# Kernel tuning notes

Measured on AMD Instinct MI355X. Metric: run time of the kernel, lower is better.

The kernel has to match this reference:

```python
import jax, jax.numpy as jnp
import numpy as np

B, A, C = 8, 150000, 10
ALPHA, GAMMA = 0.25, 2.0
STD = jnp.array([[0.1, 0.1, 0.2, 0.2]], dtype=jnp.float32)


def setup_inputs() -> dict:
    key = jax.random.key(0)
    ks = jax.random.split(key, 9)
    # ground-truth boxes (one per image), centered around (400,400)
    cx = jax.random.uniform(ks[0], (B,), minval=350., maxval=450.)
    cy = jax.random.uniform(ks[1], (B,), minval=350., maxval=450.)
    w = jax.random.uniform(ks[2], (B,), minval=80., maxval=180.)
    h = jax.random.uniform(ks[3], (B,), minval=80., maxval=180.)
    boxes = jnp.stack([cx - 0.5 * w, cy - 0.5 * h, cx + 0.5 * w, cy + 0.5 * h], axis=1)
    labels = (jax.random.uniform(ks[4], (B, C)) < 0.3).astype(jnp.float32)
    annotations = jnp.concatenate([boxes, labels], axis=1)  # [B, 4+C]
    n_near = A // 20
    kc = jax.random.split(ks[5], 4)
    ncx = jax.random.uniform(kc[0], (n_near,), minval=350., maxval=450.)
    ncy = jax.random.uniform(kc[1], (n_near,), minval=350., maxval=450.)
    nw = jax.random.uniform(kc[2], (n_near,), minval=80., maxval=180.)
    nh = jax.random.uniform(kc[3], (n_near,), minval=80., maxval=180.)
    kr = jax.random.split(ks[6], 4)
    rcx = jax.random.uniform(kr[0], (A - n_near,), minval=0., maxval=800.)
    rcy = jax.random.uniform(kr[1], (A - n_near,), minval=0., maxval=800.)
    rw = jax.random.uniform(kr[2], (A - n_near,), minval=20., maxval=300.)
    rh = jax.random.uniform(kr[3], (A - n_near,), minval=20., maxval=300.)
    acx = jnp.concatenate([ncx, rcx]); acy = jnp.concatenate([ncy, rcy])
    aw = jnp.concatenate([nw, rw]); ah = jnp.concatenate([nh, rh])
    anchors = jnp.stack([acx - 0.5 * aw, acy - 0.5 * ah, acx + 0.5 * aw, acy + 0.5 * ah], axis=1)[None]  # [1,A,4]
    attributes = jax.random.uniform(ks[7], (B, A, C), dtype=jnp.float32)  # probs in (0,1)
    regressions = jax.random.normal(ks[8], (B, A, 4), dtype=jnp.float32)
    return {"attributes": attributes, "regressions": regressions,
            "anchors": anchors, "annotations": annotations}


def reference(attributes, regressions, anchors, annotations):
    anchor = anchors[0]  # [A,4]
    aw = anchor[:, 2] - anchor[:, 0]
    ah = anchor[:, 3] - anchor[:, 1]
    acx = anchor[:, 0] + 0.5 * aw
    acy = anchor[:, 1] + 0.5 * ah

    def per_image(attribute, regression, ann):  # [A,C], [A,4], [4+C]
        box, labels = ann[:4], ann[4:]
        attribute = jnp.clip(attribute, 1e-4, 1.0 - 1e-4)
        # IoU of every anchor with the single gt box -> [A]
        area = (box[2] - box[0]) * (box[3] - box[1])
        iw = jnp.clip(jnp.minimum(anchor[:, 2], box[2]) - jnp.maximum(anchor[:, 0], box[0]), 0.0)
        ih = jnp.clip(jnp.minimum(anchor[:, 3], box[3]) - jnp.maximum(anchor[:, 1], box[1]), 0.0)
        inter = iw * ih
        union = jnp.clip(aw * ah + area - inter, 1e-8)
        iou = inter / union
        neg = iou < 0.4
        pos = iou >= 0.5
        num_pos = pos.sum()
        # classification targets: -1 ignore, 0 background, gt labels for positives
        targets = jnp.full(attribute.shape, -1.0, attribute.dtype)
        targets = jnp.where(neg[:, None], 0.0, targets)
        targets = jnp.where(pos[:, None], labels[None, :], targets)
        alpha_factor = jnp.where(targets == 1.0, ALPHA, 1.0 - ALPHA)
        focal_w = jnp.where(targets == 1.0, 1.0 - attribute, attribute)
        focal_w = alpha_factor * focal_w ** GAMMA
        bce = -(targets * jnp.log(attribute) + (1.0 - targets) * jnp.log(1.0 - attribute))
        att_loss = jnp.where(targets != -1.0, focal_w * bce, 0.0)
        att_loss = att_loss.sum() / jnp.maximum(num_pos.astype(attribute.dtype), 1.0)
        gw_raw = box[2] - box[0]; gh_raw = box[3] - box[1]
        gcx = box[0] + 0.5 * gw_raw; gcy = box[1] + 0.5 * gh_raw
        gw = jnp.clip(gw_raw, 1.0); gh = jnp.clip(gh_raw, 1.0)
        t = jnp.stack([(gcx - acx) / aw, (gcy - acy) / ah,
                       jnp.log(gw / aw), jnp.log(gh / ah)], axis=1) / STD  # [A,4]
        diff = jnp.abs(t - regression)
        rl = jnp.where(diff <= 1.0 / 9.0, 0.5 * 9.0 * diff ** 2, diff - 0.5 / 9.0)
        rl_sum = jnp.where(pos[:, None], rl, 0.0).sum()
        denom = jnp.maximum(num_pos, 1).astype(attribute.dtype) * 4.0  # mean over [P,4]
        reg_loss = jnp.where(num_pos > 0, rl_sum / denom, 0.0)
        return att_loss, reg_loss

    att_losses, reg_losses = jax.vmap(per_image)(attributes, regressions, annotations)
    return (att_losses.mean(keepdims=True), reg_losses.mean(keepdims=True))
```

## Files before the change

kernel.cpp:

```cpp
#include <hip/hip_runtime.h>

constexpr int B_IMG = 8;
constexpr int A_ANCH = 150000;
constexpr int C_CLS = 10;
constexpr int TPB = 256;
constexpr int NBX = (A_ANCH + TPB * 2 - 1) / (TPB * 2);

__global__ __launch_bounds__(TPB, 4) void focal_main(
    const float* __restrict__ attr,
    const float* __restrict__ regr,
    const float* __restrict__ anch,
    const float* __restrict__ ann,
    float* __restrict__ att_part,
    float* __restrict__ rl_part,
    float* __restrict__ np_part)
{
    const int b = blockIdx.y;
    const int a0 = (blockIdx.x * TPB + threadIdx.x) * 2;
    const bool valid = (a0 < A_ANCH);

    float4 at4[5];
    float4 an4[2];
    if (valid) {
        const float4* ap = reinterpret_cast<const float4*>(attr + ((size_t)b * A_ANCH + a0) * C_CLS);
#pragma unroll
        for (int j = 0; j < 5; ++j) at4[j] = ap[j];
        const float4* anp = reinterpret_cast<const float4*>(anch) + a0;
        an4[0] = anp[0];
        an4[1] = anp[1];
    }
    __builtin_amdgcn_sched_barrier(0);

    const float* annb = ann + b * 14;
    const float bx0 = annb[0], by0 = annb[1], bx1 = annb[2], by1 = annb[3];
    float lab[C_CLS];
#pragma unroll
    for (int c = 0; c < C_CLS; ++c) lab[c] = annb[4 + c];

    const float gw_raw = bx1 - bx0;
    const float gh_raw = by1 - by0;
    const float area = gw_raw * gh_raw;
    const float gcx = bx0 + 0.5f * gw_raw;
    const float gcy = by0 + 0.5f * gh_raw;
    const float gw = fmaxf(gw_raw, 1.0f);
    const float gh = fmaxf(gh_raw, 1.0f);

    const float TH  = (float)(1.0 / 9.0);
    const float SUB = (float)(0.5 / 9.0);
    const float PHI = (float)(1.0 - 0.0001);

    float att_sum = 0.0f;
    float rl_sum = 0.0f;
    float npf = 0.0f;

    if (valid) {
#pragma unroll
        for (int k = 0; k < 2; ++k) {
            const float ax0 = an4[k].x, ay0 = an4[k].y, ax1 = an4[k].z, ay1 = an4[k].w;
            const float aw = ax1 - ax0;
            const float ah = ay1 - ay0;
            float iw = fminf(ax1, bx1) - fmaxf(ax0, bx0);
            float ih = fminf(ay1, by1) - fmaxf(ay0, by0);
            iw = fmaxf(iw, 0.0f);
            ih = fmaxf(ih, 0.0f);
            const float inter = iw * ih;
            const float uni = fmaxf(aw * ah + area - inter, 1e-8f);
            const float iou = inter / uni;
            const bool pos = (iou >= 0.5f);
            const bool neg = (iou < 0.4f);

            if (pos || neg) {
#pragma unroll
                for (int c = 0; c < C_CLS; ++c) {
                    const int e = k * C_CLS + c;
                    const float4& v = at4[e >> 2];
                    const float pe = (e & 3) == 0 ? v.x : (e & 3) == 1 ? v.y : (e & 3) == 2 ? v.z : v.w;
                    const float p = fminf(fmaxf(pe, 1e-4f), PHI);
                    const float tgt = pos ? lab[c] : 0.0f;
                    float loss;
                    if (tgt == 1.0f) {
                        const float q = 1.0f - p;
                        loss = 0.25f * (q * q) * (-__logf(p));
                    } else {
                        loss = 0.75f * (p * p) * (-__logf(1.0f - p));
                    }
                    att_sum += loss;
                }
            }
            if (pos) {
                npf += 1.0f;
                const float acx = ax0 + 0.5f * aw;
                const float acy = ay0 + 0.5f * ah;
                const float t0 = ((gcx - acx) / aw) / 0.1f;
                const float t1 = ((gcy - acy) / ah) / 0.1f;
                const float t2 = __logf(gw / aw) / 0.2f;
                const float t3 = __logf(gh / ah) / 0.2f;
                const float4 r = *reinterpret_cast<const float4*>(regr + ((size_t)b * A_ANCH + a0 + k) * 4);
                float d;
                d = fabsf(t0 - r.x); rl_sum += (d <= TH) ? 4.5f * d * d : d - SUB;
                d = fabsf(t1 - r.y); rl_sum += (d <= TH) ? 4.5f * d * d : d - SUB;
                d = fabsf(t2 - r.z); rl_sum += (d <= TH) ? 4.5f * d * d : d - SUB;
                d = fabsf(t3 - r.w); rl_sum += (d <= TH) ? 4.5f * d * d : d - SUB;
            }
        }
    }

#pragma unroll
    for (int off = 32; off > 0; off >>= 1) {
        att_sum += __shfl_down(att_sum, off);
        rl_sum  += __shfl_down(rl_sum, off);
        npf     += __shfl_down(npf, off);
    }

    __shared__ float s_att[TPB / 64];
    __shared__ float s_rl[TPB / 64];
    __shared__ float s_np[TPB / 64];
    const int wave = threadIdx.x >> 6;
    const int lane = threadIdx.x & 63;
    if (lane == 0) { s_att[wave] = att_sum; s_rl[wave] = rl_sum; s_np[wave] = npf; }
    __syncthreads();
    if (threadIdx.x == 0) {
        float a0s = 0.0f, r0 = 0.0f, n0 = 0.0f;
#pragma unroll
        for (int w = 0; w < TPB / 64; ++w) { a0s += s_att[w]; r0 += s_rl[w]; n0 += s_np[w]; }
        const int idx = b * NBX + blockIdx.x;
        att_part[idx] = a0s;
        rl_part[idx]  = r0;
        np_part[idx]  = n0;
    }
}

__global__ __launch_bounds__(512) void focal_finalize(
    const float* __restrict__ att_part,
    const float* __restrict__ rl_part,
    const float* __restrict__ np_part,
    float* __restrict__ out)
{
    const int wave = threadIdx.x >> 6;
    const int lane = threadIdx.x & 63;
    float as = 0.0f, rs = 0.0f, ns = 0.0f;
    if (wave < B_IMG) {
        for (int i = lane; i < NBX; i += 64) {
            as += att_part[wave * NBX + i];
            rs += rl_part[wave * NBX + i];
            ns += np_part[wave * NBX + i];
        }
    }
#pragma unroll
    for (int off = 32; off > 0; off >>= 1) {
        as += __shfl_down(as, off);
        rs += __shfl_down(rs, off);
        ns += __shfl_down(ns, off);
    }
    __shared__ float sa[B_IMG], sr[B_IMG], sn[B_IMG];
    if (lane == 0 && wave < B_IMG) { sa[wave] = as; sr[wave] = rs; sn[wave] = ns; }
    __syncthreads();
    if (threadIdx.x == 0) {
        double am = 0.0, rm = 0.0;
        for (int b = 0; b < B_IMG; ++b) {
            const double npd = (double)sn[b];
            const double npf = npd > 0.0 ? npd : 1.0;
            am += (double)sa[b] / npf;
            if (npd > 0.0) rm += (double)sr[b] / (npf * 4.0);
        }
        out[0] = (float)(am / (double)B_IMG);
        out[1] = (float)(rm / (double)B_IMG);
    }
}

extern "C" void kernel_launch(void* const* d_in, const int* in_sizes, int n_in,
                              void* d_out, int out_size, void* d_ws, size_t ws_size,
                              hipStream_t stream) {
    const float* attr = (const float*)d_in[0];
    const float* regr = (const float*)d_in[1];
    const float* anch = (const float*)d_in[2];
    const float* ann  = (const float*)d_in[3];
    float* out = (float*)d_out;

    float* att_part = (float*)d_ws;
    float* rl_part  = att_part + B_IMG * NBX;
    float* np_part  = rl_part + B_IMG * NBX;

    dim3 grid(NBX, B_IMG);
    focal_main<<<grid, TPB, 0, stream>>>(attr, regr, anch, ann, att_part, rl_part, np_part);
    focal_finalize<<<1, 512, 0, stream>>>(att_part, rl_part, np_part, out);
}
```

Before: 23.52 us.

## Process four images per block with software-prefetched attribute loads

Each thread now handles the same two anchors across four images, loading the anchor boxes once and reusing their derived geometry. Attribute loads for the next image are double-buffered so they are in flight while the current image is computed. The block-level shared-memory reduction is dropped in favour of per-wave partial sums, and the finalize kernel reads the larger partial buffer. This cuts the grid to a quarter of its former size and raises register pressure, which may lower occupancy.

```diff
diff --git a/kernel.cpp b/kernel.cpp
--- a/kernel.cpp
+++ b/kernel.cpp
@@ -4,9 +4,14 @@
 constexpr int A_ANCH = 150000;
 constexpr int C_CLS = 10;
 constexpr int TPB = 256;
-constexpr int NBX = (A_ANCH + TPB * 2 - 1) / (TPB * 2);
-
-__global__ __launch_bounds__(TPB, 4) void focal_main(
+constexpr int BA = TPB * 2;
+constexpr int NBX = (A_ANCH + BA - 1) / BA;
+constexpr int IPG = 4;
+constexpr int NGRP = B_IMG / IPG;
+constexpr int WPB = TPB / 64;
+constexpr int SEG = NBX * WPB;
+
+__global__ __launch_bounds__(TPB) void focal_main(
     const float* __restrict__ attr,
     const float* __restrict__ regr,
     const float* __restrict__ anch,
@@ -15,118 +20,143 @@
     float* __restrict__ rl_part,
     float* __restrict__ np_part)
 {
-    const int b = blockIdx.y;
-    const int a0 = (blockIdx.x * TPB + threadIdx.x) * 2;
+    const int g   = blockIdx.y;
+    const int b0  = g * IPG;
+    const int tid = threadIdx.x;
+    const int a0  = (blockIdx.x * TPB + tid) * 2;
     const bool valid = (a0 < A_ANCH);
-
-    float4 at4[5];
-    float4 an4[2];
-    if (valid) {
-        const float4* ap = reinterpret_cast<const float4*>(attr + ((size_t)b * A_ANCH + a0) * C_CLS);
-#pragma unroll
-        for (int j = 0; j < 5; ++j) at4[j] = ap[j];
-        const float4* anp = reinterpret_cast<const float4*>(anch) + a0;
-        an4[0] = anp[0];
-        an4[1] = anp[1];
-    }
-    __builtin_amdgcn_sched_barrier(0);
-
-    const float* annb = ann + b * 14;
-    const float bx0 = annb[0], by0 = annb[1], bx1 = annb[2], by1 = annb[3];
-    float lab[C_CLS];
-#pragma unroll
-    for (int c = 0; c < C_CLS; ++c) lab[c] = annb[4 + c];
-
-    const float gw_raw = bx1 - bx0;
-    const float gh_raw = by1 - by0;
-    const float area = gw_raw * gh_raw;
-    const float gcx = bx0 + 0.5f * gw_raw;
-    const float gcy = by0 + 0.5f * gh_raw;
-    const float gw = fmaxf(gw_raw, 1.0f);
-    const float gh = fmaxf(gh_raw, 1.0f);
 
     const float TH  = (float)(1.0 / 9.0);
     const float SUB = (float)(0.5 / 9.0);
     const float PHI = (float)(1.0 - 0.0001);
 
-    float att_sum = 0.0f;
-    float rl_sum = 0.0f;
-    float npf = 0.0f;
+    float att[IPG], rl[IPG], npf[IPG];
+#pragma unroll
+    for (int i = 0; i < IPG; ++i) { att[i] = 0.0f; rl[i] = 0.0f; npf[i] = 0.0f; }
 
     if (valid) {
-#pragma unroll
-        for (int k = 0; k < 2; ++k) {
-            const float ax0 = an4[k].x, ay0 = an4[k].y, ax1 = an4[k].z, ay1 = an4[k].w;
-            const float aw = ax1 - ax0;
-            const float ah = ay1 - ay0;
-            float iw = fminf(ax1, bx1) - fmaxf(ax0, bx0);
-            float ih = fminf(ay1, by1) - fmaxf(ay0, by0);
-            iw = fmaxf(iw, 0.0f);
-            ih = fmaxf(ih, 0.0f);
-            const float inter = iw * ih;
-            const float uni = fmaxf(aw * ah + area - inter, 1e-8f);
-            const float iou = inter / uni;
-            const bool pos = (iou >= 0.5f);
-            const bool neg = (iou < 0.4f);
-
-            if (pos || neg) {
-#pragma unroll
-                for (int c = 0; c < C_CLS; ++c) {
-                    const int e = k * C_CLS + c;
-                    const float4& v = at4[e >> 2];
-                    const float pe = (e & 3) == 0 ? v.x : (e & 3) == 1 ? v.y : (e & 3) == 2 ? v.z : v.w;
-                    const float p = fminf(fmaxf(pe, 1e-4f), PHI);
-                    const float tgt = pos ? lab[c] : 0.0f;
-                    float loss;
-                    if (tgt == 1.0f) {
-                        const float q = 1.0f - p;
-                        loss = 0.25f * (q * q) * (-__logf(p));
-                    } else {
-                        loss = 0.75f * (p * p) * (-__logf(1.0f - p));
+        const float4* anp = reinterpret_cast<const float4*>(anch) + a0;
+        const float4 anA = anp[0];
+        const float4 anB = anp[1];
+        float ax1[2], ay1[2], aw[2], ah[2], acx[2], acy[2], aarea[2];
+        {
+            const float4 an[2] = {anA, anB};
+#pragma unroll
+            for (int k = 0; k < 2; ++k) {
+                ax1[k] = an[k].z; ay1[k] = an[k].w;
+                aw[k] = an[k].z - an[k].x;
+                ah[k] = an[k].w - an[k].y;
+                acx[k] = an[k].x + 0.5f * aw[k];
+                acy[k] = an[k].y + 0.5f * ah[k];
+                aarea[k] = aw[k] * ah[k];
+            }
+        }
+        const float ax0v[2] = {anA.x, anB.x};
+        const float ay0v[2] = {anA.y, anB.y};
+
+        const size_t f4row0 = (((size_t)b0 * A_ANCH + a0) * C_CLS) >> 2;
+        const size_t f4stride = ((size_t)A_ANCH * C_CLS) >> 2;
+        const float4* atp = reinterpret_cast<const float4*>(attr);
+
+        float4 bufA[5], bufB[5];
+#pragma unroll
+        for (int j = 0; j < 5; ++j) bufA[j] = atp[f4row0 + j];
+
+        auto body = [&](const int i, float4 (&cur)[5], float4 (&nxt)[5],
+                        const bool prefetch, float& att_i, float& rl_i, float& np_i) {
+            const int b = b0 + i;
+            if (prefetch) {
+#pragma unroll
+                for (int j = 0; j < 5; ++j) nxt[j] = atp[f4row0 + (size_t)(i + 1) * f4stride + j];
+            }
+            const float* annb = ann + b * 14;
+            const float bx0 = annb[0], by0 = annb[1], bx1 = annb[2], by1 = annb[3];
+            float lab[C_CLS];
+#pragma unroll
+            for (int c = 0; c < C_CLS; ++c) lab[c] = annb[4 + c];
+
+            const float gw_raw = bx1 - bx0;
+            const float gh_raw = by1 - by0;
+            const float area = gw_raw * gh_raw;
+            const float gcx = bx0 + 0.5f * gw_raw;
+            const float gcy = by0 + 0.5f * gh_raw;
+            const float gw = fmaxf(gw_raw, 1.0f);
+            const float gh = fmaxf(gh_raw, 1.0f);
+
+#pragma unroll
+            for (int k = 0; k < 2; ++k) {
+                float iw = fminf(ax1[k], bx1) - fmaxf(ax0v[k], bx0);
+                float ih = fminf(ay1[k], by1) - fmaxf(ay0v[k], by0);
+                iw = fmaxf(iw, 0.0f);
+                ih = fmaxf(ih, 0.0f);
+                const float inter = iw * ih;
+                const float uni = fmaxf(aarea[k] + area - inter, 1e-8f);
+                const float iou = inter / uni;
+                const bool pos = (iou >= 0.5f);
+                const bool neg = (iou < 0.4f);
+
+                if (pos || neg) {
+#pragma unroll
+                    for (int c = 0; c < C_CLS; ++c) {
+                        const int e = k * C_CLS + c;
+                        const float4& v = cur[e >> 2];
+                        const float pe = (e & 3) == 0 ? v.x : (e & 3) == 1 ? v.y
+                                       : (e & 3) == 2 ? v.z : v.w;
+                        const float p = fminf(fmaxf(pe, 1e-4f), PHI);
+                        const float tgt = pos ? lab[c] : 0.0f;
+                        float loss;
+                        if (tgt == 1.0f) {
+                            const float q = 1.0f - p;
+                            loss = 0.25f * (q * q) * (-__logf(p));
+                        } else {
+                            loss = 0.75f * (p * p) * (-__logf(1.0f - p));
+                        }
+                        att_i += loss;
                     }
-                    att_sum += loss;
+                }
+                if (pos) {
+                    np_i += 1.0f;
+                    const float t0 = ((gcx - acx[k]) / aw[k]) / 0.1f;
+                    const float t1 = ((gcy - acy[k]) / ah[k]) / 0.1f;
+                    const float t2 = __logf(gw / aw[k]) / 0.2f;
+                    const float t3 = __logf(gh / ah[k]) / 0.2f;
+                    const float4 r = *reinterpret_cast<const float4*>(
+                        regr + ((size_t)b * A_ANCH + a0 + k) * 4);
+                    float d;
+                    d = fabsf(t0 - r.x); rl_i += (d <= TH) ? 4.5f * d * d : d - SUB;
+                    d = fabsf(t1 - r.y); rl_i += (d <= TH) ? 4.5f * d * d : d - SUB;
+                    d = fabsf(t2 - r.z); rl_i += (d <= TH) ? 4.5f * d * d : d - SUB;
+                    d = fabsf(t3 - r.w); rl_i += (d <= TH) ? 4.5f * d * d : d - SUB;
                 }
             }
-            if (pos) {
-                npf += 1.0f;
-                const float acx = ax0 + 0.5f * aw;
-                const float acy = ay0 + 0.5f * ah;
-                const float t0 = ((gcx - acx) / aw) / 0.1f;
-                const float t1 = ((gcy - acy) / ah) / 0.1f;
-                const float t2 = __logf(gw / aw) / 0.2f;
-                const float t3 = __logf(gh / ah) / 0.2f;
-                const float4 r = *reinterpret_cast<const float4*>(regr + ((size_t)b * A_ANCH + a0 + k) * 4);
-                float d;
-                d = fabsf(t0 - r.x); rl_sum += (d <= TH) ? 4.5f * d * d : d - SUB;
-                d = fabsf(t1 - r.y); rl_sum += (d <= TH) ? 4.5f * d * d : d - SUB;
-                d = fabsf(t2 - r.z); rl_sum += (d <= TH) ? 4.5f * d * d : d - SUB;
-                d = fabsf(t3 - r.w); rl_sum += (d <= TH) ? 4.5f * d * d : d - SUB;
-            }
-        }
+        };
+
+        body(0, bufA, bufB, true,  att[0], rl[0], npf[0]);
+        body(1, bufB, bufA, true,  att[1], rl[1], npf[1]);
+        body(2, bufA, bufB, true,  att[2], rl[2], npf[2]);
+        body(3, bufB, bufA, false, att[3], rl[3], npf[3]);
     }
 
 #pragma unroll
     for (int off = 32; off > 0; off >>= 1) {
-        att_sum += __shfl_down(att_sum, off);
-        rl_sum  += __shfl_down(rl_sum, off);
-        npf     += __shfl_down(npf, off);
-    }
-
-    __shared__ float s_att[TPB / 64];
-    __shared__ float s_rl[TPB / 64];
-    __shared__ float s_np[TPB / 64];
-    const int wave = threadIdx.x >> 6;
-    const int lane = threadIdx.x & 63;
-    if (lane == 0) { s_att[wave] = att_sum; s_rl[wave] = rl_sum; s_np[wave] = npf; }
-    __syncthreads();
-    if (threadIdx.x == 0) {
-        float a0s = 0.0f, r0 = 0.0f, n0 = 0.0f;
-#pragma unroll
-        for (int w = 0; w < TPB / 64; ++w) { a0s += s_att[w]; r0 += s_rl[w]; n0 += s_np[w]; }
-        const int idx = b * NBX + blockIdx.x;
-        att_part[idx] = a0s;
-        rl_part[idx]  = r0;
-        np_part[idx]  = n0;
+#pragma unroll
+        for (int i = 0; i < IPG; ++i) {
+            att[i] += __shfl_down(att[i], off);
+            rl[i]  += __shfl_down(rl[i], off);
+            npf[i] += __shfl_down(npf[i], off);
+        }
+    }
+    const int wave = tid >> 6;
+    const int lane = tid & 63;
+    if (lane == 0) {
+        const int widx = blockIdx.x * WPB + wave;
+#pragma unroll
+        for (int i = 0; i < IPG; ++i) {
+            const int idx = (b0 + i) * SEG + widx;
+            att_part[idx] = att[i];
+            rl_part[idx]  = rl[i];
+            np_part[idx]  = npf[i];
+        }
     }
 }
 
@@ -140,10 +170,10 @@
     const int lane = threadIdx.x & 63;
     float as = 0.0f, rs = 0.0f, ns = 0.0f;
     if (wave < B_IMG) {
-        for (int i = lane; i < NBX; i += 64) {
-            as += att_part[wave * NBX + i];
-            rs += rl_part[wave * NBX + i];
-            ns += np_part[wave * NBX + i];
+        for (int i = lane; i < SEG; i += 64) {
+            as += att_part[wave * SEG + i];
+            rs += rl_part[wave * SEG + i];
+            ns += np_part[wave * SEG + i];
         }
     }
 #pragma unroll
@@ -159,9 +189,9 @@
         double am = 0.0, rm = 0.0;
         for (int b = 0; b < B_IMG; ++b) {
             const double npd = (double)sn[b];
-            const double npf = npd > 0.0 ? npd : 1.0;
-            am += (double)sa[b] / npf;
-            if (npd > 0.0) rm += (double)sr[b] / (npf * 4.0);
+            const double den = npd > 0.0 ? npd : 1.0;
+            am += (double)sa[b] / den;
+            if (npd > 0.0) rm += (double)sr[b] / (den * 4.0);
         }
         out[0] = (float)(am / (double)B_IMG);
         out[1] = (float)(rm / (double)B_IMG);
@@ -178,10 +208,10 @@
     float* out = (float*)d_out;
 
     float* att_part = (float*)d_ws;
-    float* rl_part  = att_part + B_IMG * NBX;
-    float* np_part  = rl_part + B_IMG * NBX;
-
-    dim3 grid(NBX, B_IMG);
+    float* rl_part  = att_part + B_IMG * SEG;
+    float* np_part  = rl_part + B_IMG * SEG;
+
+    dim3 grid(NBX, NGRP);
     focal_main<<<grid, TPB, 0, stream>>>(attr, regr, anch, ann, att_part, rl_part, np_part);
     focal_finalize<<<1, 512, 0, stream>>>(att_part, rl_part, np_part, out);
 }
```

Result: slower. 32.06 us (+36.3%).
